# Kernel optimization log

Hardware: AMD Instinct MI355X
Metric: run time of the kernel (lower is better)

Reference implementation:

```python
import jax, jax.numpy as jnp
import numpy as np

G = 2   # FlipGroup order
H = 16  # num_heads
TEMPERATURE = 1.0


def _shared_w(A, B):
    # Z2 regular-representation equivariant linear: block-circulant weight
    # W = [[A, B], [B, A]], shape (dim, dim)
    return jnp.concatenate([
        jnp.concatenate([A, B], axis=1),
        jnp.concatenate([B, A], axis=1),
    ], axis=0)


def setup_inputs() -> dict:
    key = jax.random.key(0)
    ks = jax.random.split(key, 9)
    d = 1024
    dh = d // G
    inp = {"x": jax.random.normal(ks[0], (4, 1024, d), jnp.float32)}
    for i, n in enumerate(["wqA", "wqB", "wkA", "wkB", "wvA", "wvB", "wpA", "wpB"]):
        inp[n] = jax.random.normal(ks[i + 1], (dh, dh), jnp.float32) * 0.02
    return inp


def reference(x, wqA, wqB, wkA, wkB, wvA, wvB, wpA, wpB):
    B, N, C = x.shape
    hd = C // G // H            # per-group-channel head dim
    scale = hd ** -0.5

    q = x @ _shared_w(wqA, wqB).T
    k = x @ _shared_w(wkA, wkB).T
    v = x @ _shared_w(wvA, wvB).T

    def split(t):
        # (B,N,C) -> (B,H,G,N,hd): per-head features split into G group channels
        return t.reshape(B, N, H, G, hd).transpose(0, 2, 3, 1, 4)

    q, k, v = split(q), split(k), split(v)

    # per-channel attention: independent softmax per (head, group-channel)
    attn = jax.nn.softmax(
        jnp.einsum('bhgnd,bhgmd->bhgnm', q, k) * (scale / TEMPERATURE), axis=-1)
    o = jnp.einsum('bhgnm,bhgmd->bhgnd', attn, v)

    o = o.transpose(0, 3, 1, 2, 4).reshape(B, N, C)
    return o @ _shared_w(wpA, wpB).T
```

## Files before the change

### kernel.cpp

```cpp
#include <hip/hip_runtime.h>


typedef unsigned short ushort_t;
typedef __attribute__((ext_vector_type(4))) unsigned short ushort4_t;
typedef __attribute__((ext_vector_type(8))) unsigned short ushort8;
typedef __attribute__((ext_vector_type(8))) __bf16 bf16x8;
typedef __attribute__((ext_vector_type(4))) float f32x4;
typedef __attribute__((ext_vector_type(4))) unsigned int uint4_t;

#define GPTR(p) ((const __attribute__((address_space(1))) void*)(p))
#define LPTR(p) ((__attribute__((address_space(3))) void*)(p))

static __device__ __forceinline__ unsigned short f2b(float f) {
  unsigned int u = __builtin_bit_cast(unsigned int, f);
  unsigned int r = u + 0x7fffu + ((u >> 16) & 1u);
  return (unsigned short)(r >> 16);
}
static __device__ __forceinline__ float b2f(ushort_t h) {
  unsigned int u = ((unsigned int)h) << 16;
  return __builtin_bit_cast(float, u);
}
static __device__ __forceinline__ unsigned int pack_rtna(float a, float b) {
  const unsigned int ua = (__builtin_bit_cast(unsigned int, a) + 0x8000u) >> 16;
  const unsigned int ub = (__builtin_bit_cast(unsigned int, b) + 0x8000u) & 0xFFFF0000u;
  return ub | ua;
}

__global__ __launch_bounds__(256) void prep_k(
    const float* __restrict__ x,
    const float* __restrict__ wqA, const float* __restrict__ wqB,
    const float* __restrict__ wkA, const float* __restrict__ wkB,
    const float* __restrict__ wvA, const float* __restrict__ wvB,
    const float* __restrict__ wpA, const float* __restrict__ wpB,
    ushort_t* __restrict__ xsd, ushort_t* __restrict__ Wsd,
    ushort_t* __restrict__ Wp, float sclq) {
  const int bid = blockIdx.x;
  if (bid < 1024) {
    const int u = bid * 256 + threadIdx.x;
    const int m = u >> 6;
    const int k8 = (u & 63) * 8;
    const float* p1 = x + (size_t)m * 1024 + k8;
    const float* p2 = p1 + 512;
    const f32x4 a0 = *(const f32x4*)p1,  a1 = *(const f32x4*)(p1 + 4);
    const f32x4 b0 = *(const f32x4*)p2,  b1 = *(const f32x4*)(p2 + 4);
    ushort8 vs, vd;
#pragma unroll
    for (int e = 0; e < 4; ++e) {
      vs[e] = f2b(a0[e] + b0[e]); vs[e + 4] = f2b(a1[e] + b1[e]);
      vd[e] = f2b(a0[e] - b0[e]); vd[e + 4] = f2b(a1[e] - b1[e]);
    }
    *(ushort8*)&xsd[(size_t)m * 1024 + k8] = vs;
    *(ushort8*)&xsd[(size_t)m * 1024 + 512 + k8] = vd;
  } else if (bid < 1792) {
    const int u = (bid - 1024) * 256 + threadIdx.x;
    const int hm = u >> 15;
    const int rem = u & 32767;
    const int r = rem >> 6;
    const int c8 = (rem & 63) * 8;
    const int proj = hm >> 1, isD = hm & 1;
    const float* A; const float* B;
    if (proj == 0)      { A = wqA; B = wqB; }
    else if (proj == 1) { A = wkA; B = wkB; }
    else                { A = wvA; B = wvB; }
    const float scl = 0.5f * (proj == 0 ? sclq : 1.0f);
    const f32x4 a0 = *(const f32x4*)(A + (size_t)r * 512 + c8);
    const f32x4 a1 = *(const f32x4*)(A + (size_t)r * 512 + c8 + 4);
    const f32x4 b0 = *(const f32x4*)(B + (size_t)r * 512 + c8);
    const f32x4 b1 = *(const f32x4*)(B + (size_t)r * 512 + c8 + 4);
    ushort8 v;
#pragma unroll
    for (int e = 0; e < 4; ++e) {
      v[e]     = f2b(isD ? (a0[e] - b0[e]) * scl : (a0[e] + b0[e]) * scl);
      v[e + 4] = f2b(isD ? (a1[e] - b1[e]) * scl : (a1[e] + b1[e]) * scl);
    }
    *(ushort8*)&Wsd[(size_t)(proj * 1024 + isD * 512 + r) * 512 + c8] = v;
  } else {
    const int u = (bid - 1792) * 256 + threadIdx.x;
    const int r = u >> 7;
    const int cc = (u & 127) * 8;
    const float* src = (((r ^ cc) & 512) ? wpB : wpA) + (size_t)(r & 511) * 512 + (cc & 511);
    const f32x4 a = *(const f32x4*)src;
    const f32x4 b = *(const f32x4*)(src + 4);
    ushort8 v;
#pragma unroll
    for (int e = 0; e < 4; ++e) { v[e] = f2b(a[e]); v[e + 4] = f2b(b[e]); }
    *(ushort8*)&Wp[(size_t)r * 1024 + cc] = v;
  }
}

__global__ __launch_bounds__(512, 2) void gemm_sd_qkv(const ushort_t* __restrict__ xsd,
                                                      const ushort_t* __restrict__ Wsd,
                                                      ushort_t* __restrict__ Qb,
                                                      ushort_t* __restrict__ Kb,
                                                      ushort_t* __restrict__ Vtb) {
  __shared__ ushort_t sh[73728];

  const int t = threadIdx.x;
  const int wid = t >> 6, lane = t & 63;
  const int wm = wid >> 2, wn = wid & 3;
  const int half = wn >> 1;
  const int lr = lane & 15, lg = lane >> 4;

  const int bid = blockIdx.x;
  const int c = bid & 7, j = bid >> 3;
  const int mt = (c >> 1) * 4 + (j & 3);
  const int nzt = (c & 1) * 6 + (j >> 2);
  const int z = nzt >> 2;
  const int n0 = (nzt & 3) * 128;
  const int m0 = mt * 256;

  f32x4 acc[8][4];
  const f32x4 fz = {0.f, 0.f, 0.f, 0.f};
#pragma unroll
  for (int mf = 0; mf < 8; ++mf)
#pragma unroll
    for (int nf = 0; nf < 4; ++nf) acc[mf][nf] = fz;

#define ISSUE(kt_, s_)                                                                   \
  {                                                                                      \
    ushort_t* base_ = sh + (s_) * 24576;                                                 \
    const int k0_ = (kt_) * 32;                                                          \
    _Pragma("unroll") for (int rnd = 0; rnd < 2; ++rnd) {                                \
      const int ch = rnd * 512 + t;                                                      \
      const int row = ch >> 2, cs = ch & 3;                                              \
      const int gcol = k0_ + ((cs ^ ((row >> 1) & 3)) << 3);                             \
      __builtin_amdgcn_global_load_lds(GPTR(xsd + (size_t)(m0 + row) * 1024 + gcol),     \
                                       LPTR(base_ + (size_t)ch * 8), 16, 0, 0);          \
      __builtin_amdgcn_global_load_lds(GPTR(xsd + (size_t)(m0 + row) * 1024 + 512 + gcol),\
                                       LPTR(base_ + 8192 + (size_t)ch * 8), 16, 0, 0);   \
    }                                                                                    \
    {                                                                                    \
      const int row = t >> 2, cs = t & 3;                                                \
      const int gcol = k0_ + ((cs ^ ((row >> 1) & 3)) << 3);                             \
      __builtin_amdgcn_global_load_lds(                                                  \
          GPTR(Wsd + (size_t)(z * 1024 + n0 + row) * 512 + gcol),                        \
          LPTR(base_ + 16384 + (size_t)t * 8), 16, 0, 0);                                \
      __builtin_amdgcn_global_load_lds(                                                  \
          GPTR(Wsd + (size_t)(z * 1024 + 512 + n0 + row) * 512 + gcol),                  \
          LPTR(base_ + 20480 + (size_t)t * 8), 16, 0, 0);                                \
    }                                                                                    \
  }

  ISSUE(0, 0) ISSUE(1, 1)
  int s = 0;
  for (int kt = 0; kt < 16; ++kt) {
    asm volatile("" ::: "memory");
    __builtin_amdgcn_s_barrier();
    asm volatile("" ::: "memory");
    if (kt < 14) {
      const int s2 = (s >= 1) ? s - 1 : 2;
      ISSUE(kt + 2, s2)
      asm volatile("s_waitcnt vmcnt(12)" ::: "memory");
    } else if (kt == 14) {
      asm volatile("s_waitcnt vmcnt(6)" ::: "memory");
    } else {
      asm volatile("s_waitcnt vmcnt(0)" ::: "memory");
    }
    __builtin_amdgcn_sched_barrier(0);
    __builtin_amdgcn_s_barrier();
    asm volatile("" ::: "memory");

    const ushort_t* base = sh + s * 24576;
    const ushort_t* Asl = base + half * 8192;
    const ushort_t* Bsl = base + 16384 + half * 4096;
    bf16x8 a[8], b[4];
#pragma unroll
    for (int mf = 0; mf < 8; ++mf) {
      const int row = wm * 128 + mf * 16 + lr;
      a[mf] = *(const bf16x8*)&Asl[row * 32 + ((lg ^ ((row >> 1) & 3)) << 3)];
    }
#pragma unroll
    for (int nf = 0; nf < 4; ++nf) {
      const int row = (wn & 1) * 64 + nf * 16 + lr;
      b[nf] = *(const bf16x8*)&Bsl[row * 32 + ((lg ^ ((row >> 1) & 3)) << 3)];
    }
    __builtin_amdgcn_s_setprio(1);
#pragma unroll
    for (int mf = 0; mf < 8; ++mf)
#pragma unroll
      for (int nf = 0; nf < 4; ++nf)
        acc[mf][nf] = __builtin_amdgcn_mfma_f32_16x16x32_bf16(a[mf], b[nf], acc[mf][nf], 0, 0, 0);
    __builtin_amdgcn_s_setprio(0);
    s = (s == 2) ? 0 : s + 1;
  }
#undef ISSUE

  __syncthreads();
  const int PAD = (z < 2) ? 136 : 137;
  ushort_t* tus = sh;
  ushort_t* tvd = sh + 256 * PAD;
  {
    ushort_t* dst = half ? tvd : tus;
#pragma unroll
    for (int mf = 0; mf < 8; ++mf)
#pragma unroll
      for (int nf = 0; nf < 4; ++nf)
#pragma unroll
        for (int rr = 0; rr < 4; ++rr) {
          const int row = wm * 128 + mf * 16 + lg * 4 + rr;
          const int col = (wn & 1) * 64 + nf * 16 + lr;
          dst[row * PAD + col] = f2b(acc[mf][nf][rr]);
        }
  }
  __syncthreads();

  if (z < 2) {
    ushort_t* C = (z == 0) ? Qb : Kb;
#pragma unroll
    for (int it = 0; it < 8; ++it) {
      const int idx = it * 512 + t;
      const int row = idx >> 4;
      const int c8 = (idx & 15) * 8;
      const ushort8 u8 = *(const ushort8*)&tus[row * 136 + c8];
      const ushort8 v8 = *(const ushort8*)&tvd[row * 136 + c8];
      ushort8 y1, y2;
#pragma unroll
      for (int e = 0; e < 8; ++e) {
        const float us = b2f(u8[e]), vd = b2f(v8[e]);
        y1[e] = f2b(us + vd);
        y2[e] = f2b(us - vd);
      }
      *(ushort8*)&C[(size_t)(m0 + row) * 1024 + n0 + c8] = y1;
      *(ushort8*)&C[(size_t)(m0 + row) * 1024 + 512 + n0 + c8] = y2;
    }
  } else {
    const int bidx = m0 >> 10, tok0 = m0 & 1023;
#pragma unroll
    for (int it = 0; it < 8; ++it) {
      const int idx = it * 512 + t;
      const int cr = idx >> 5;
      const int mc = (idx & 31) * 8;
      float y1v[8], y2v[8];
#pragma unroll
      for (int e = 0; e < 8; ++e) {
        const float us = b2f(tus[(mc + e) * 137 + cr]);
        const float vd = b2f(tvd[(mc + e) * 137 + cr]);
        y1v[e] = us + vd;
        y2v[e] = us - vd;
      }
      const int k6 = mc & 63;
      const int base = (k6 & 0x20) | ((k6 & 8) << 1) | ((k6 & 0x10) >> 2);
      const size_t rb1 = (size_t)bidx * 1024 * 1024 + (size_t)(n0 + cr) * 1024 +
                         tok0 + (mc & ~63) + base;
      const size_t rb2 = (size_t)bidx * 1024 * 1024 + (size_t)(512 + n0 + cr) * 1024 +
                         tok0 + (mc & ~63) + base;
      ushort4_t lo1, hi1, lo2, hi2;
#pragma unroll
      for (int e = 0; e < 4; ++e) {
        lo1[e] = f2b(y1v[e]); hi1[e] = f2b(y1v[e + 4]);
        lo2[e] = f2b(y2v[e]); hi2[e] = f2b(y2v[e + 4]);
      }
      *(ushort4_t*)&Vtb[rb1] = lo1;  *(ushort4_t*)&Vtb[rb1 + 8] = hi1;
      *(ushort4_t*)&Vtb[rb2] = lo2;  *(ushort4_t*)&Vtb[rb2 + 8] = hi2;
    }
  }
}

__global__ __launch_bounds__(256) void gemm_out(const ushort_t* __restrict__ Ob,
                                                const ushort_t* __restrict__ Wp,
                                                float* __restrict__ out) {
  __shared__ ushort_t sh[24576];
  const int nlin = blockIdx.x;
  const int c = nlin & 7, j = nlin >> 3;
  const int xt = j & 7, yt = c * 4 + (j >> 3);
  const int m0 = yt * 128, n0 = xt * 128;
  const int t = threadIdx.x;
  const int w = t >> 6, lane = t & 63;
  const int wr = w >> 1, wc = w & 1;
  const int lr = lane & 15, lg = lane >> 4;
  const int rkey = (lr >> 1) & 3;
  f32x4 acc[4][4];
  const f32x4 fz = {0.f, 0.f, 0.f, 0.f};
#pragma unroll
  for (int i = 0; i < 4; ++i)
#pragma unroll
    for (int jj = 0; jj < 4; ++jj) acc[i][jj] = fz;

#define ISSUE_O(kt_, s_)                                                                 \
  {                                                                                      \
    ushort_t* As_ = sh + (s_) * 8192;                                                    \
    ushort_t* Bs_ = As_ + 4096;                                                          \
    _Pragma("unroll") for (int rnd = 0; rnd < 2; ++rnd) {                                \
      const int ch = rnd * 256 + t;                                                      \
      const int row = ch >> 2, kc = ch & 3;                                              \
      const int gcol = (kt_) * 32 + ((kc ^ ((row >> 1) & 3)) << 3);                      \
      __builtin_amdgcn_global_load_lds(GPTR(Ob + (size_t)(m0 + row) * 1024 + gcol),      \
                                       LPTR(As_ + (size_t)ch * 8), 16, 0, 0);            \
      __builtin_amdgcn_global_load_lds(GPTR(Wp + (size_t)(n0 + row) * 1024 + gcol),      \
                                       LPTR(Bs_ + (size_t)ch * 8), 16, 0, 0);            \
    }                                                                                    \
  }

  ISSUE_O(0, 0) ISSUE_O(1, 1)
  int s = 0;
  for (int kt = 0; kt < 32; ++kt) {
    asm volatile("" ::: "memory");
    __builtin_amdgcn_s_barrier();
    asm volatile("" ::: "memory");
    if (kt < 30) {
      const int s2 = (s >= 1) ? s - 1 : 2;
      ISSUE_O(kt + 2, s2)
      asm volatile("s_waitcnt vmcnt(8)" ::: "memory");
    } else if (kt == 30) {
      asm volatile("s_waitcnt vmcnt(4)" ::: "memory");
    } else {
      asm volatile("s_waitcnt vmcnt(0)" ::: "memory");
    }
    __builtin_amdgcn_sched_barrier(0);
    __builtin_amdgcn_s_barrier();
    asm volatile("" ::: "memory");

    const ushort_t* As = sh + s * 8192;
    const ushort_t* Bs = As + 4096;
    bf16x8 a[4], b[4];
#pragma unroll
    for (int i = 0; i < 4; ++i)
      a[i] = *(const bf16x8*)&As[(wr * 64 + i * 16 + lr) * 32 + ((lg ^ rkey) << 3)];
#pragma unroll
    for (int jj = 0; jj < 4; ++jj)
      b[jj] = *(const bf16x8*)&Bs[(wc * 64 + jj * 16 + lr) * 32 + ((lg ^ rkey) << 3)];
    __builtin_amdgcn_s_setprio(1);
#pragma unroll
    for (int i = 0; i < 4; ++i)
#pragma unroll
      for (int jj = 0; jj < 4; ++jj)
        acc[i][jj] = __builtin_amdgcn_mfma_f32_16x16x32_bf16(a[i], b[jj], acc[i][jj], 0, 0, 0);
    __builtin_amdgcn_s_setprio(0);
    s = (s == 2) ? 0 : s + 1;
  }
#undef ISSUE_O

#pragma unroll
  for (int i = 0; i < 4; ++i)
#pragma unroll
    for (int jj = 0; jj < 4; ++jj)
#pragma unroll
      for (int r = 0; r < 4; ++r) {
        const int rg = m0 + wr * 64 + i * 16 + lg * 4 + r;
        const int cg = n0 + wc * 64 + jj * 16 + lr;
        out[(size_t)rg * 1024 + cg] = acc[i][jj][r];
      }
}

__global__ __launch_bounds__(256, 4) void attn_k(const ushort_t* __restrict__ Q,
                                                 const ushort_t* __restrict__ K,
                                                 const ushort_t* __restrict__ Vt,
                                                 ushort_t* __restrict__ O) {
  __shared__ ushort_t KsL[4 * 2048];
  __shared__ ushort_t VsL[4 * 2048];
  const int t = threadIdx.x;
  const int w = t >> 6, lane = t & 63;
  const int lr = lane & 15, lg = lane >> 4, lk8 = lg * 8;
  const int rkey = (lr >> 1) & 3;
  const int pkey = lr & 7;

  const int nlin = blockIdx.x;
  const int c = nlin & 7, j = nlin >> 3;
  const int p = c * 16 + (j >> 3);
  const int qb = j & 7;
  const int hh = p & 31, b = p >> 5;

  const size_t bbase = (size_t)b * 1024 * 1024;
  const size_t headc = (size_t)hh * 32;
  const size_t vtbase = ((size_t)b * 1024 + hh * 32) * 1024;
  const int q0 = qb * 128 + w * 32;
  const f32x4 fzero = {0.f, 0.f, 0.f, 0.f};

  bf16x8 bq[2];
#pragma unroll
  for (int i = 0; i < 2; ++i)
    bq[i] = *(const bf16x8*)&Q[bbase + (size_t)(q0 + i * 16 + lr) * 1024 + headc + lk8];

  f32x4 oacc[2][2];
  float tq[2] = {0.f, 0.f};
#pragma unroll
  for (int i = 0; i < 2; ++i)
#pragma unroll
    for (int jj = 0; jj < 2; ++jj) oacc[i][jj] = fzero;

#define ISSUE_KV(kt_, s_)                                                                \
  {                                                                                      \
    ushort_t* Kd_ = KsL + (s_) * 2048;                                                   \
    ushort_t* Vd_ = VsL + (s_) * 2048;                                                   \
    const int krow = t >> 2, kc = t & 3;                                                 \
    __builtin_amdgcn_global_load_lds(                                                    \
        GPTR(K + bbase + (size_t)((kt_) * 64 + krow) * 1024 + headc +                    \
             ((kc ^ ((krow >> 1) & 3)) << 3)),                                           \
        LPTR(Kd_ + (size_t)t * 8), 16, 0, 0);                                            \
    const int vrow = t >> 3, vc = t & 7;                                                 \
    __builtin_amdgcn_global_load_lds(                                                    \
        GPTR(Vt + vtbase + (size_t)vrow * 1024 + (kt_) * 64 + ((vc ^ (vrow & 7)) << 3)), \
        LPTR(Vd_ + (size_t)t * 8), 16, 0, 0);                                            \
  }

  ISSUE_KV(0, 0) ISSUE_KV(1, 1) ISSUE_KV(2, 2)
  for (int kt = 0; kt < 16; ++kt) {
    const int s = kt & 3;
    asm volatile("" ::: "memory");
    __builtin_amdgcn_s_barrier();
    asm volatile("" ::: "memory");
    if (kt < 13) {
      ISSUE_KV(kt + 3, (kt + 3) & 3)
      asm volatile("s_waitcnt vmcnt(6)" ::: "memory");
    } else if (kt == 13) {
      asm volatile("s_waitcnt vmcnt(4)" ::: "memory");
    } else if (kt == 14) {
      asm volatile("s_waitcnt vmcnt(2)" ::: "memory");
    } else {
      asm volatile("s_waitcnt vmcnt(0)" ::: "memory");
    }
    __builtin_amdgcn_sched_barrier(0);
    __builtin_amdgcn_s_barrier();
    asm volatile("" ::: "memory");

    const ushort_t* Ksb = KsL + s * 2048;
    const ushort_t* Vsb = VsL + s * 2048;

    bf16x8 ak[4];
#pragma unroll
    for (int kf = 0; kf < 4; ++kf)
      ak[kf] = *(const bf16x8*)&Ksb[(kf * 16 + lr) * 32 + ((lg ^ rkey) << 3)];

    bf16x8 ap[2][2];
#pragma unroll
    for (int i = 0; i < 2; ++i) {
      f32x4 s4[4];
      __builtin_amdgcn_s_setprio(1);
#pragma unroll
      for (int kf = 0; kf < 4; ++kf)
        s4[kf] = __builtin_amdgcn_mfma_f32_16x16x32_bf16(ak[kf], bq[i], fzero, 0, 0, 0);
      __builtin_amdgcn_s_setprio(0);
#pragma unroll
      for (int ks = 0; ks < 2; ++ks) {
        const float p0 = __builtin_amdgcn_exp2f(s4[2 * ks][0]);
        const float p1 = __builtin_amdgcn_exp2f(s4[2 * ks][1]);
        const float p2 = __builtin_amdgcn_exp2f(s4[2 * ks][2]);
        const float p3 = __builtin_amdgcn_exp2f(s4[2 * ks][3]);
        const float p4 = __builtin_amdgcn_exp2f(s4[2 * ks + 1][0]);
        const float p5 = __builtin_amdgcn_exp2f(s4[2 * ks + 1][1]);
        const float p6 = __builtin_amdgcn_exp2f(s4[2 * ks + 1][2]);
        const float p7 = __builtin_amdgcn_exp2f(s4[2 * ks + 1][3]);
        tq[i] += ((p0 + p1) + (p2 + p3)) + ((p4 + p5) + (p6 + p7));
        uint4_t u;
        u[0] = pack_rtna(p0, p1);
        u[1] = pack_rtna(p2, p3);
        u[2] = pack_rtna(p4, p5);
        u[3] = pack_rtna(p6, p7);
        ap[i][ks] = __builtin_bit_cast(bf16x8, u);
      }
    }

#pragma unroll
    for (int ks = 0; ks < 2; ++ks) {
      bf16x8 bv0 = *(const bf16x8*)&Vsb[(0 * 16 + lr) * 64 + ((ks * 32 + lk8) ^ (pkey << 3))];
      bf16x8 bv1 = *(const bf16x8*)&Vsb[(1 * 16 + lr) * 64 + ((ks * 32 + lk8) ^ (pkey << 3))];
      __builtin_amdgcn_s_setprio(1);
#pragma unroll
      for (int i = 0; i < 2; ++i) {
        oacc[i][0] = __builtin_amdgcn_mfma_f32_16x16x32_bf16(ap[i][ks], bv0, oacc[i][0], 0, 0, 0);
        oacc[i][1] = __builtin_amdgcn_mfma_f32_16x16x32_bf16(ap[i][ks], bv1, oacc[i][1], 0, 0, 0);
      }
      __builtin_amdgcn_s_setprio(0);
    }
  }
#undef ISSUE_KV

#pragma unroll
  for (int i = 0; i < 2; ++i) {
    tq[i] += __shfl_xor(tq[i], 16, 64);
    tq[i] += __shfl_xor(tq[i], 32, 64);
  }

#pragma unroll
  for (int i = 0; i < 2; ++i) {
    float inv[4];
#pragma unroll
    for (int r = 0; r < 4; ++r)
      inv[r] = 1.0f / __shfl(tq[i], lg * 4 + r, 64);
#pragma unroll
    for (int jj = 0; jj < 2; ++jj)
#pragma unroll
      for (int r = 0; r < 4; ++r)
        O[bbase + (size_t)(q0 + i * 16 + lg * 4 + r) * 1024 + headc + jj * 16 + lr] =
            f2b(oacc[i][jj][r] * inv[r]);
  }
}

extern "C" void kernel_launch(void* const* d_in, const int* in_sizes, int n_in,
                              void* d_out, int out_size, void* d_ws, size_t ws_size,
                              hipStream_t stream) {
  const float* x   = (const float*)d_in[0];
  const float* wqA = (const float*)d_in[1];
  const float* wqB = (const float*)d_in[2];
  const float* wkA = (const float*)d_in[3];
  const float* wkB = (const float*)d_in[4];
  const float* wvA = (const float*)d_in[5];
  const float* wvB = (const float*)d_in[6];
  const float* wpA = (const float*)d_in[7];
  const float* wpB = (const float*)d_in[8];
  float* out = (float*)d_out;

  const size_t NE = (size_t)4096 * 1024;
  ushort_t* Qb   = (ushort_t*)d_ws;
  ushort_t* Kb   = Qb + NE;
  ushort_t* Vtb  = Kb + NE;
  ushort_t* xsd  = Vtb + NE;
  ushort_t* Wsd  = xsd + NE;
  ushort_t* Wp   = Wsd + (size_t)3072 * 512;
  ushort_t* Ob   = xsd;

  const float SCL = 0.17677669529663687f * 1.4426950408889634f;

  prep_k<<<2304, 256, 0, stream>>>(x, wqA, wqB, wkA, wkB, wvA, wvB, wpA, wpB,
                                   xsd, Wsd, Wp, SCL);
  gemm_sd_qkv<<<192, 512, 0, stream>>>(xsd, Wsd, Qb, Kb, Vtb);
  attn_k<<<1024, 256, 0, stream>>>(Qb, Kb, Vtb, Ob);
  gemm_out<<<256, 256, 0, stream>>>(Ob, Wp, out);

  (void)in_sizes; (void)n_in; (void)out_size; (void)ws_size;
}
```

Before: 87.10 us.

## Apply sum/difference block-diagonalization to output projection fused into attention epilogue

Result: faster. 82.71 us (-5.0%).

```diff
diff --git a/kernel.cpp b/kernel.cpp
--- a/kernel.cpp
+++ b/kernel.cpp
@@ -32,8 +32,7 @@
     const float* __restrict__ wkA, const float* __restrict__ wkB,
     const float* __restrict__ wvA, const float* __restrict__ wvB,
     const float* __restrict__ wpA, const float* __restrict__ wpB,
-    ushort_t* __restrict__ xsd, ushort_t* __restrict__ Wsd,
-    ushort_t* __restrict__ Wp, float sclq) {
+    ushort_t* __restrict__ xsd, ushort_t* __restrict__ Wsd, float sclq) {
   const int bid = blockIdx.x;
   if (bid < 1024) {
     const int u = bid * 256 + threadIdx.x;
@@ -51,7 +50,7 @@
     }
     *(ushort8*)&xsd[(size_t)m * 1024 + k8] = vs;
     *(ushort8*)&xsd[(size_t)m * 1024 + 512 + k8] = vd;
-  } else if (bid < 1792) {
+  } else {
     const int u = (bid - 1024) * 256 + threadIdx.x;
     const int hm = u >> 15;
     const int rem = u & 32767;
@@ -61,7 +60,8 @@
     const float* A; const float* B;
     if (proj == 0)      { A = wqA; B = wqB; }
     else if (proj == 1) { A = wkA; B = wkB; }
-    else                { A = wvA; B = wvB; }
+    else if (proj == 2) { A = wvA; B = wvB; }
+    else                { A = wpA; B = wpB; }
     const float scl = 0.5f * (proj == 0 ? sclq : 1.0f);
     const f32x4 a0 = *(const f32x4*)(A + (size_t)r * 512 + c8);
     const f32x4 a1 = *(const f32x4*)(A + (size_t)r * 512 + c8 + 4);
@@ -74,17 +74,6 @@
       v[e + 4] = f2b(isD ? (a1[e] - b1[e]) * scl : (a1[e] + b1[e]) * scl);
     }
     *(ushort8*)&Wsd[(size_t)(proj * 1024 + isD * 512 + r) * 512 + c8] = v;
-  } else {
-    const int u = (bid - 1792) * 256 + threadIdx.x;
-    const int r = u >> 7;
-    const int cc = (u & 127) * 8;
-    const float* src = (((r ^ cc) & 512) ? wpB : wpA) + (size_t)(r & 511) * 512 + (cc & 511);
-    const f32x4 a = *(const f32x4*)src;
-    const f32x4 b = *(const f32x4*)(src + 4);
-    ushort8 v;
-#pragma unroll
-    for (int e = 0; e < 4; ++e) { v[e] = f2b(a[e]); v[e + 4] = f2b(b[e]); }
-    *(ushort8*)&Wp[(size_t)r * 1024 + cc] = v;
   }
 }
 
@@ -256,114 +245,31 @@
   }
 }
 
-__global__ __launch_bounds__(256) void gemm_out(const ushort_t* __restrict__ Ob,
-                                                const ushort_t* __restrict__ Wp,
-                                                float* __restrict__ out) {
-  __shared__ ushort_t sh[24576];
-  const int nlin = blockIdx.x;
-  const int c = nlin & 7, j = nlin >> 3;
-  const int xt = j & 7, yt = c * 4 + (j >> 3);
-  const int m0 = yt * 128, n0 = xt * 128;
+__global__ __launch_bounds__(512, 4) void attn_k(const ushort_t* __restrict__ Q,
+                                                 const ushort_t* __restrict__ K,
+                                                 const ushort_t* __restrict__ Vt,
+                                                 ushort_t* __restrict__ Osd) {
+  __shared__ ushort_t shmem[32768];
+  ushort_t* KsL = shmem;
+  ushort_t* VsL = shmem + 16384;
+  float* obuf = (float*)shmem;
+
   const int t = threadIdx.x;
   const int w = t >> 6, lane = t & 63;
-  const int wr = w >> 1, wc = w & 1;
-  const int lr = lane & 15, lg = lane >> 4;
-  const int rkey = (lr >> 1) & 3;
-  f32x4 acc[4][4];
-  const f32x4 fz = {0.f, 0.f, 0.f, 0.f};
-#pragma unroll
-  for (int i = 0; i < 4; ++i)
-#pragma unroll
-    for (int jj = 0; jj < 4; ++jj) acc[i][jj] = fz;
-
-#define ISSUE_O(kt_, s_)                                                                 \
-  {                                                                                      \
-    ushort_t* As_ = sh + (s_) * 8192;                                                    \
-    ushort_t* Bs_ = As_ + 4096;                                                          \
-    _Pragma("unroll") for (int rnd = 0; rnd < 2; ++rnd) {                                \
-      const int ch = rnd * 256 + t;                                                      \
-      const int row = ch >> 2, kc = ch & 3;                                              \
-      const int gcol = (kt_) * 32 + ((kc ^ ((row >> 1) & 3)) << 3);                      \
-      __builtin_amdgcn_global_load_lds(GPTR(Ob + (size_t)(m0 + row) * 1024 + gcol),      \
-                                       LPTR(As_ + (size_t)ch * 8), 16, 0, 0);            \
-      __builtin_amdgcn_global_load_lds(GPTR(Wp + (size_t)(n0 + row) * 1024 + gcol),      \
-                                       LPTR(Bs_ + (size_t)ch * 8), 16, 0, 0);            \
-    }                                                                                    \
-  }
-
-  ISSUE_O(0, 0) ISSUE_O(1, 1)
-  int s = 0;
-  for (int kt = 0; kt < 32; ++kt) {
-    asm volatile("" ::: "memory");
-    __builtin_amdgcn_s_barrier();
-    asm volatile("" ::: "memory");
-    if (kt < 30) {
-      const int s2 = (s >= 1) ? s - 1 : 2;
-      ISSUE_O(kt + 2, s2)
-      asm volatile("s_waitcnt vmcnt(8)" ::: "memory");
-    } else if (kt == 30) {
-      asm volatile("s_waitcnt vmcnt(4)" ::: "memory");
-    } else {
-      asm volatile("s_waitcnt vmcnt(0)" ::: "memory");
-    }
-    __builtin_amdgcn_sched_barrier(0);
-    __builtin_amdgcn_s_barrier();
-    asm volatile("" ::: "memory");
-
-    const ushort_t* As = sh + s * 8192;
-    const ushort_t* Bs = As + 4096;
-    bf16x8 a[4], b[4];
-#pragma unroll
-    for (int i = 0; i < 4; ++i)
-      a[i] = *(const bf16x8*)&As[(wr * 64 + i * 16 + lr) * 32 + ((lg ^ rkey) << 3)];
-#pragma unroll
-    for (int jj = 0; jj < 4; ++jj)
-      b[jj] = *(const bf16x8*)&Bs[(wc * 64 + jj * 16 + lr) * 32 + ((lg ^ rkey) << 3)];
-    __builtin_amdgcn_s_setprio(1);
-#pragma unroll
-    for (int i = 0; i < 4; ++i)
-#pragma unroll
-      for (int jj = 0; jj < 4; ++jj)
-        acc[i][jj] = __builtin_amdgcn_mfma_f32_16x16x32_bf16(a[i], b[jj], acc[i][jj], 0, 0, 0);
-    __builtin_amdgcn_s_setprio(0);
-    s = (s == 2) ? 0 : s + 1;
-  }
-#undef ISSUE_O
-
-#pragma unroll
-  for (int i = 0; i < 4; ++i)
-#pragma unroll
-    for (int jj = 0; jj < 4; ++jj)
-#pragma unroll
-      for (int r = 0; r < 4; ++r) {
-        const int rg = m0 + wr * 64 + i * 16 + lg * 4 + r;
-        const int cg = n0 + wc * 64 + jj * 16 + lr;
-        out[(size_t)rg * 1024 + cg] = acc[i][jj][r];
-      }
-}
-
-__global__ __launch_bounds__(256, 4) void attn_k(const ushort_t* __restrict__ Q,
-                                                 const ushort_t* __restrict__ K,
-                                                 const ushort_t* __restrict__ Vt,
-                                                 ushort_t* __restrict__ O) {
-  __shared__ ushort_t KsL[4 * 2048];
-  __shared__ ushort_t VsL[4 * 2048];
-  const int t = threadIdx.x;
-  const int w = t >> 6, lane = t & 63;
+  const int hw = w >> 2;
   const int lr = lane & 15, lg = lane >> 4, lk8 = lg * 8;
   const int rkey = (lr >> 1) & 3;
   const int pkey = lr & 7;
 
   const int nlin = blockIdx.x;
   const int c = nlin & 7, j = nlin >> 3;
-  const int p = c * 16 + (j >> 3);
+  const int p = c * 8 + (j >> 3);
   const int qb = j & 7;
-  const int hh = p & 31, b = p >> 5;
+  const int hp = p & 15, b = p >> 4;
 
   const size_t bbase = (size_t)b * 1024 * 1024;
-  const size_t headc = (size_t)hh * 32;
-  const size_t vtbase = ((size_t)b * 1024 + hh * 32) * 1024;
-  const int q0 = qb * 128 + w * 32;
+  const size_t headc = (size_t)hp * 32 + hw * 512;
+  const int q0 = qb * 128 + (w & 3) * 32;
   const f32x4 fzero = {0.f, 0.f, 0.f, 0.f};
 
   bf16x8 bq[2];
@@ -380,16 +286,19 @@
 
 #define ISSUE_KV(kt_, s_)                                                                \
   {                                                                                      \
-    ushort_t* Kd_ = KsL + (s_) * 2048;                                                   \
-    ushort_t* Vd_ = VsL + (s_) * 2048;                                                   \
-    const int krow = t >> 2, kc = t & 3;                                                 \
+    ushort_t* Kd_ = KsL + (s_) * 4096;                                                   \
+    ushort_t* Vd_ = VsL + (s_) * 4096;                                                   \
+    const int hl = t >> 8, rem = t & 255;                                                \
+    const size_t hc_ = (size_t)hp * 32 + hl * 512;                                       \
+    const int krow = rem >> 2, kc = rem & 3;                                             \
     __builtin_amdgcn_global_load_lds(                                                    \
-        GPTR(K + bbase + (size_t)((kt_) * 64 + krow) * 1024 + headc +                    \
+        GPTR(K + bbase + (size_t)((kt_) * 64 + krow) * 1024 + hc_ +                      \
              ((kc ^ ((krow >> 1) & 3)) << 3)),                                           \
         LPTR(Kd_ + (size_t)t * 8), 16, 0, 0);                                            \
-    const int vrow = t >> 3, vc = t & 7;                                                 \
+    const int vrow = rem >> 3, vc = rem & 7;                                             \
     __builtin_amdgcn_global_load_lds(                                                    \
-        GPTR(Vt + vtbase + (size_t)vrow * 1024 + (kt_) * 64 + ((vc ^ (vrow & 7)) << 3)), \
+        GPTR(Vt + bbase + (size_t)(hc_ + vrow) * 1024 + (kt_) * 64 +                     \
+             ((vc ^ (vrow & 7)) << 3)),                                                  \
         LPTR(Vd_ + (size_t)t * 8), 16, 0, 0);                                            \
   }
 
@@ -413,8 +322,8 @@
     __builtin_amdgcn_s_barrier();
     asm volatile("" ::: "memory");
 
-    const ushort_t* Ksb = KsL + s * 2048;
-    const ushort_t* Vsb = VsL + s * 2048;
+    const ushort_t* Ksb = KsL + s * 4096 + hw * 2048;
+    const ushort_t* Vsb = VsL + s * 4096 + hw * 2048;
 
     bf16x8 ak[4];
 #pragma unroll
@@ -471,6 +380,7 @@
     tq[i] += __shfl_xor(tq[i], 32, 64);
   }
 
+  __syncthreads();
 #pragma unroll
   for (int i = 0; i < 2; ++i) {
     float inv[4];
@@ -480,9 +390,151 @@
 #pragma unroll
     for (int jj = 0; jj < 2; ++jj)
 #pragma unroll
-      for (int r = 0; r < 4; ++r)
-        O[bbase + (size_t)(q0 + i * 16 + lg * 4 + r) * 1024 + headc + jj * 16 + lr] =
-            f2b(oacc[i][jj][r] * inv[r]);
+      for (int r = 0; r < 4; ++r) {
+        const int row = (w & 3) * 32 + i * 16 + lg * 4 + r;
+        obuf[hw * 4224 + row * 33 + jj * 16 + lr] = oacc[i][jj][r] * inv[r];
+      }
+  }
+  __syncthreads();
+
+  {
+    const int row = t >> 2;
+    const int c8 = (t & 3) * 8;
+    ushort8 vs, vd;
+#pragma unroll
+    for (int e = 0; e < 8; ++e) {
+      const float o0 = obuf[0 * 4224 + row * 33 + c8 + e];
+      const float o1 = obuf[1 * 4224 + row * 33 + c8 + e];
+      vs[e] = f2b(o0 + o1);
+      vd[e] = f2b(o0 - o1);
+    }
+    const size_t rowg = bbase + (size_t)(qb * 128 + row) * 1024;
+    *(ushort8*)&Osd[rowg + hp * 32 + c8] = vs;
+    *(ushort8*)&Osd[rowg + 512 + hp * 32 + c8] = vd;
+  }
+}
+
+__global__ __launch_bounds__(256, 4) void gemm_out_sd(const ushort_t* __restrict__ Osd,
+                                                      const ushort_t* __restrict__ Wsd,
+                                                      float* __restrict__ out) {
+  __shared__ ushort_t sh[36864];
+
+  const int t = threadIdx.x;
+  const int w = t >> 6, lane = t & 63;
+  const int wm = w >> 1, half = w & 1;
+  const int lr = lane & 15, lg = lane >> 4;
+
+  const int bid = blockIdx.x;
+  const int c = bid & 7, j = bid >> 3;
+  const int mt = c * 4 + (j & 3);
+  const int st = j >> 2;
+  const int m0 = mt * 128, n0s = st * 64;
+
+  f32x4 acc[4][4];
+  const f32x4 fz = {0.f, 0.f, 0.f, 0.f};
+#pragma unroll
+  for (int mf = 0; mf < 4; ++mf)
+#pragma unroll
+    for (int nf = 0; nf < 4; ++nf) acc[mf][nf] = fz;
+
+#define ISSUE_O(kt_, s_)                                                                 \
+  {                                                                                      \
+    ushort_t* base_ = sh + (s_) * 12288;                                                 \
+    const int k0_ = (kt_) * 32;                                                          \
+    _Pragma("unroll") for (int rnd = 0; rnd < 2; ++rnd) {                                \
+      const int ch = rnd * 256 + t;                                                      \
+      const int row = ch >> 2, kc = ch & 3;                                              \
+      const int gcol = k0_ + ((kc ^ ((row >> 1) & 3)) << 3);                             \
+      __builtin_amdgcn_global_load_lds(GPTR(Osd + (size_t)(m0 + row) * 1024 + gcol),     \
+                                       LPTR(base_ + (size_t)ch * 8), 16, 0, 0);          \
+      __builtin_amdgcn_global_load_lds(GPTR(Osd + (size_t)(m0 + row) * 1024 + 512 + gcol),\
+                                       LPTR(base_ + 4096 + (size_t)ch * 8), 16, 0, 0);   \
+    }                                                                                    \
+    {                                                                                    \
+      const int row = t >> 2, kc = t & 3;                                                \
+      const int gcol = k0_ + ((kc ^ ((row >> 1) & 3)) << 3);                             \
+      __builtin_amdgcn_global_load_lds(                                                  \
+          GPTR(Wsd + (size_t)(3072 + n0s + row) * 512 + gcol),                           \
+          LPTR(base_ + 8192 + (size_t)t * 8), 16, 0, 0);                                 \
+      __builtin_amdgcn_global_load_lds(                                                  \
+          GPTR(Wsd + (size_t)(3072 + 512 + n0s + row) * 512 + gcol),                     \
+          LPTR(base_ + 10240 + (size_t)t * 8), 16, 0, 0);                                \
+    }                                                                                    \
+  }
+
+  ISSUE_O(0, 0) ISSUE_O(1, 1)
+  int s = 0;
+  for (int kt = 0; kt < 16; ++kt) {
+    asm volatile("" ::: "memory");
+    __builtin_amdgcn_s_barrier();
+    asm volatile("" ::: "memory");
+    if (kt < 14) {
+      const int s2 = (s >= 1) ? s - 1 : 2;
+      ISSUE_O(kt + 2, s2)
+      asm volatile("s_waitcnt vmcnt(12)" ::: "memory");
+    } else if (kt == 14) {
+      asm volatile("s_waitcnt vmcnt(6)" ::: "memory");
+    } else {
+      asm volatile("s_waitcnt vmcnt(0)" ::: "memory");
+    }
+    __builtin_amdgcn_sched_barrier(0);
+    __builtin_amdgcn_s_barrier();
+    asm volatile("" ::: "memory");
+
+    const ushort_t* base = sh + s * 12288;
+    const ushort_t* Asl = base + half * 4096;
+    const ushort_t* Bsl = base + 8192 + half * 2048;
+    bf16x8 a[4], b[4];
+#pragma unroll
+    for (int mf = 0; mf < 4; ++mf) {
+      const int row = wm * 64 + mf * 16 + lr;
+      a[mf] = *(const bf16x8*)&Asl[row * 32 + ((lg ^ ((row >> 1) & 3)) << 3)];
+    }
+#pragma unroll
+    for (int nf = 0; nf < 4; ++nf) {
+      const int row = nf * 16 + lr;
+      b[nf] = *(const bf16x8*)&Bsl[row * 32 + ((lg ^ ((row >> 1) & 3)) << 3)];
+    }
+    __builtin_amdgcn_s_setprio(1);
+#pragma unroll
+    for (int mf = 0; mf < 4; ++mf)
+#pragma unroll
+      for (int nf = 0; nf < 4; ++nf)
+        acc[mf][nf] = __builtin_amdgcn_mfma_f32_16x16x32_bf16(a[mf], b[nf], acc[mf][nf], 0, 0, 0);
+    __builtin_amdgcn_s_setprio(0);
+    s = (s == 2) ? 0 : s + 1;
+  }
+#undef ISSUE_O
+
+  __syncthreads();
+  float* vdbuf = (float*)sh;
+  if (half == 1) {
+#pragma unroll
+    for (int mf = 0; mf < 4; ++mf)
+#pragma unroll
+      for (int nf = 0; nf < 4; ++nf)
+#pragma unroll
+        for (int rr = 0; rr < 4; ++rr) {
+          const int row = wm * 64 + mf * 16 + lg * 4 + rr;
+          const int col = nf * 16 + lr;
+          vdbuf[row * 66 + col] = acc[mf][nf][rr];
+        }
+  }
+  __syncthreads();
+  if (half == 0) {
+#pragma unroll
+    for (int mf = 0; mf < 4; ++mf)
+#pragma unroll
+      for (int nf = 0; nf < 4; ++nf)
+#pragma unroll
+        for (int rr = 0; rr < 4; ++rr) {
+          const int row = wm * 64 + mf * 16 + lg * 4 + rr;
+          const int col = nf * 16 + lr;
+          const float us = acc[mf][nf][rr];
+          const float vd = vdbuf[row * 66 + col];
+          out[(size_t)(m0 + row) * 1024 + n0s + col] = us + vd;
+          out[(size_t)(m0 + row) * 1024 + 512 + n0s + col] = us - vd;
+        }
   }
 }
 
@@ -506,16 +558,15 @@
   ushort_t* Vtb  = Kb + NE;
   ushort_t* xsd  = Vtb + NE;
   ushort_t* Wsd  = xsd + NE;
-  ushort_t* Wp   = Wsd + (size_t)3072 * 512;
-  ushort_t* Ob   = xsd;
+  ushort_t* Osd  = xsd;
 
   const float SCL = 0.17677669529663687f * 1.4426950408889634f;
 
-  prep_k<<<2304, 256, 0, stream>>>(x, wqA, wqB, wkA, wkB, wvA, wvB, wpA, wpB,
-                                   xsd, Wsd, Wp, SCL);
+  prep_k<<<2048, 256, 0, stream>>>(x, wqA, wqB, wkA, wkB, wvA, wvB, wpA, wpB,
+                                   xsd, Wsd, SCL);
   gemm_sd_qkv<<<192, 512, 0, stream>>>(xsd, Wsd, Qb, Kb, Vtb);
-  attn_k<<<1024, 256, 0, stream>>>(Qb, Kb, Vtb, Ob);
-  gemm_out<<<256, 256, 0, stream>>>(Ob, Wp, out);
+  attn_k<<<512, 512, 0, stream>>>(Qb, Kb, Vtb, Osd);
+  gemm_out_sd<<<256, 256, 0, stream>>>(Osd, Wsd, out);
 
   (void)in_sizes; (void)n_in; (void)out_size; (void)ws_size;
 }
```
